# Optimization experiments

Hardware: AMD Instinct MI355X
Metric: run time of the kernel (lower is better)

The kernel has to match this reference:

```python
import jax, jax.numpy as jnp
import numpy as np

B, T, TM, D, H, FF = 4, 1024, 1024, 1024, 16, 4096
HS = D // H
EPS = 1e-5


def _layer_norm(x, g, b):
    m = jnp.mean(x, axis=-1, keepdims=True)
    v = jnp.mean(jnp.square(x - m), axis=-1, keepdims=True)
    return (x - m) / jnp.sqrt(v + EPS) * g + b


def _mha(q_in, k_in, v_in, wq, bq, wk, bk, wv, bv, wo, bo):
    b, t, c = q_in.shape
    tm = k_in.shape[1]
    q = (q_in @ wq + bq).reshape(b, t, H, HS).transpose(0, 2, 1, 3)   # [b,h,t,hs]
    k = (k_in @ wk + bk).reshape(b, tm, H, HS).transpose(0, 2, 1, 3)  # [b,h,tm,hs]
    v = (v_in @ wv + bv).reshape(b, tm, H, HS).transpose(0, 2, 1, 3)
    att = jnp.einsum('bhtd,bhsd->bhts', q, k) * (1.0 / np.sqrt(HS))
    att = jax.nn.softmax(att, axis=-1)                                # [b,h,t,tm]
    y = jnp.einsum('bhts,bhsd->bhtd', att, v)
    y = y.transpose(0, 2, 1, 3).reshape(b, t, c)
    y = y @ wo + bo
    return y, att.mean(axis=1)                                        # attn avg over heads


def setup_inputs() -> dict:
    key = jax.random.key(0)
    ks = jax.random.split(key, 32)
    s = 0.02
    w = lambda k, shape: (jax.random.normal(k, shape, jnp.float32) * s)
    inp = {
        'tgt': jax.random.normal(ks[0], (B, T, D), jnp.float32),
        'memory': jax.random.normal(ks[1], (B, TM, D), jnp.float32),
        # self-attention params
        'sa_wq': w(ks[2], (D, D)), 'sa_bq': jnp.zeros((D,), jnp.float32),
        'sa_wk': w(ks[3], (D, D)), 'sa_bk': jnp.zeros((D,), jnp.float32),
        'sa_wv': w(ks[4], (D, D)), 'sa_bv': jnp.zeros((D,), jnp.float32),
        'sa_wo': w(ks[5], (D, D)), 'sa_bo': jnp.zeros((D,), jnp.float32),
        # cross-attention params
        'ca_wq': w(ks[6], (D, D)), 'ca_bq': jnp.zeros((D,), jnp.float32),
        'ca_wk': w(ks[7], (D, D)), 'ca_bk': jnp.zeros((D,), jnp.float32),
        'ca_wv': w(ks[8], (D, D)), 'ca_bv': jnp.zeros((D,), jnp.float32),
        'ca_wo': w(ks[9], (D, D)), 'ca_bo': jnp.zeros((D,), jnp.float32),
        # FFN
        'w1': w(ks[10], (D, FF)), 'b1': jnp.zeros((FF,), jnp.float32),
        'w2': w(ks[11], (FF, D)), 'b2': jnp.zeros((D,), jnp.float32),
        # LayerNorms
        'ln1_g': jnp.ones((D,), jnp.float32), 'ln1_b': jnp.zeros((D,), jnp.float32),
        'ln2_g': jnp.ones((D,), jnp.float32), 'ln2_b': jnp.zeros((D,), jnp.float32),
        'ln3_g': jnp.ones((D,), jnp.float32), 'ln3_b': jnp.zeros((D,), jnp.float32),
    }
    return inp


def reference(tgt, memory,
              sa_wq, sa_bq, sa_wk, sa_bk, sa_wv, sa_bv, sa_wo, sa_bo,
              ca_wq, ca_bq, ca_wk, ca_bk, ca_wv, ca_bv, ca_wo, ca_bo,
              w1, b1, w2, b2,
              ln1_g, ln1_b, ln2_g, ln2_b, ln3_g, ln3_b):
    x = tgt
    tmp, _ = _mha(x, x, x, sa_wq, sa_bq, sa_wk, sa_bk, sa_wv, sa_bv, sa_wo, sa_bo)
    x = _layer_norm(x + tmp, ln1_g, ln1_b)
    tmp, attention = _mha(x, memory, memory,
                          ca_wq, ca_bq, ca_wk, ca_bk, ca_wv, ca_bv, ca_wo, ca_bo)
    x = _layer_norm(x + tmp, ln2_g, ln2_b)
    tmp = jax.nn.relu(x @ w1 + b1) @ w2 + b2
    x = _layer_norm(x + tmp, ln3_g, ln3_b)
    return x, attention
```

## Files before the change

### kernel.cpp

```cpp
#include <hip/hip_runtime.h>
#include <hip/hip_bf16.h>
#include <cstdint>
#include <cstddef>

using u16 = unsigned short;
typedef __attribute__((ext_vector_type(4))) float f32x4;
typedef __attribute__((ext_vector_type(8))) short bf16x8;
typedef __attribute__((ext_vector_type(4))) short bf16x4;

constexpr int Bc = 4, Tc = 1024, TMc = 1024, Dc = 1024, Hc = 16, HSc = 64, FFc = 4096;
constexpr int BT = Bc * Tc;

struct Ptr4 { u16* p0; u16* p1; u16* p2; u16* p3; };

__device__ __forceinline__ u16 f2bf(float f) {
  union { float f; uint32_t u; } v; v.f = f;
  uint32_t u = v.u;
  u += 0x7fffu + ((u >> 16) & 1u);
  return (u16)(u >> 16);
}
__device__ __forceinline__ u16 f2bf_tr(float f) {
  union { float f; uint32_t u; } v; v.f = f;
  return (u16)(v.u >> 16);
}
__device__ __forceinline__ float b2f(u16 u) {
  union { float f; uint32_t u32; } v; v.u32 = (uint32_t)u << 16; return v.f;
}

__device__ __forceinline__ bf16x8 cat8(bf16x4 lo, bf16x4 hi) {
  bf16x8 r;
  r[0] = lo[0]; r[1] = lo[1]; r[2] = lo[2]; r[3] = lo[3];
  r[4] = hi[0]; r[5] = hi[1]; r[6] = hi[2]; r[7] = hi[3];
  return r;
}

__device__ __forceinline__ void gload16(const u16* g, u16* l) {
  __builtin_amdgcn_global_load_lds((const __attribute__((address_space(1))) void*)g,
                                   (__attribute__((address_space(3))) void*)l, 16, 0, 0);
}

__global__ __launch_bounds__(256)
void tconv(const float* __restrict__ in, u16* __restrict__ outp, int K, int N)
{
  __shared__ u16 tile[64][65];
  const int tx = threadIdx.x & 15, ty = threadIdx.x >> 4;
  const int kb = blockIdx.y * 64, nb = blockIdx.x * 64;
  #pragma unroll
  for (int i = 0; i < 4; ++i) {
    const int r = ty + i * 16;
    const float4 v = *(const float4*)(in + (size_t)(kb + r) * N + nb + tx * 4);
    tile[r][tx * 4 + 0] = f2bf(v.x);
    tile[r][tx * 4 + 1] = f2bf(v.y);
    tile[r][tx * 4 + 2] = f2bf(v.z);
    tile[r][tx * 4 + 3] = f2bf(v.w);
  }
  __syncthreads();
  #pragma unroll
  for (int i = 0; i < 4; ++i) {
    const int n = ty + i * 16;
    bf16x4 o;
    o[0] = (short)tile[tx * 4 + 0][n];
    o[1] = (short)tile[tx * 4 + 1][n];
    o[2] = (short)tile[tx * 4 + 2][n];
    o[3] = (short)tile[tx * 4 + 3][n];
    *(bf16x4*)(outp + (size_t)(nb + n) * K + kb + tx * 4) = o;
  }
}

__global__ __launch_bounds__(256)
void cvt_bf16(const float* __restrict__ in, u16* __restrict__ outp, int n4)
{
  const int i = blockIdx.x * 256 + threadIdx.x;
  if (i < n4) {
    const float4 v = ((const float4*)in)[i];
    bf16x4 o;
    o[0] = (short)f2bf(v.x); o[1] = (short)f2bf(v.y);
    o[2] = (short)f2bf(v.z); o[3] = (short)f2bf(v.w);
    ((bf16x4*)outp)[i] = o;
  }
}

template<int MODE, int BMv, int DEPTH>
__global__ __launch_bounds__((BMv == 256) ? 512 : 256)
void gemm_bt(const u16* __restrict__ A, const u16* __restrict__ Bt,
             const float* __restrict__ bias, const float* __restrict__ resid,
             void* __restrict__ outp, int M, int N, int K, int Kch, Ptr4 P)
{
  constexpr int BM = BMv, BN = 128, BK = 32;
  constexpr int NTHR = (BM == 256) ? 512 : 256;
  constexpr int RPC = NTHR / 4;
  constexpr int ACALLS = BM / RPC;
  constexpr int BCALLS = BN / RPC;
  constexpr int CALLS = ACALLS + BCALLS;
  constexpr int NB = DEPTH + 1;
  __shared__ __align__(16) u16 As[NB][BM * BK];
  __shared__ __align__(16) u16 Bs[NB][BN * BK];
  const int tid = threadIdx.x;
  const int lane = tid & 63, w = tid >> 6;
  const int wr = w >> 1, wc = w & 1;
  const int hi4 = lane >> 4, lr = lane & 15;

  const int nwg = gridDim.x;
  const int GX = N / BN;
  const int bid0 = (int)blockIdx.x;
  const int L = (bid0 & 7) * (nwg >> 3) + (bid0 >> 3);
  const int bandw = 8 * GX;
  const int band = L / bandw;
  const int rem = L - band * bandw;
  const int m0 = (band * 8 + (rem & 7)) * BM;
  const int n0 = (rem >> 3) * BN;

  const int k0 = (MODE == 3) ? (int)blockIdx.y * Kch : 0;

  const int srow = tid >> 2;
  const int gslot = (tid & 3) ^ ((srow >> 1) & 3);
  const u16* ga = A  + (size_t)(m0 + srow) * K + k0 + gslot * 8;
  const u16* gb = Bt + (size_t)(n0 + srow) * K + k0 + gslot * 8;
  const int wofs = w * 512;
  const int cswz = (lr >> 1) & 3;

  auto stage = [&](int buf, int kt) {
    #pragma unroll
    for (int j = 0; j < ACALLS; ++j)
      gload16(ga + (size_t)j * RPC * K + kt, &As[buf][j * NTHR * 8 + wofs]);
    #pragma unroll
    for (int j = 0; j < BCALLS; ++j)
      gload16(gb + (size_t)j * RPC * K + kt, &Bs[buf][j * NTHR * 8 + wofs]);
  };

  f32x4 acc[4][4] = {};
  const int nt = Kch / BK;

  #pragma unroll
  for (int p = 0; p < DEPTH; ++p)
    if (p < nt) stage(p % NB, p * BK);

  int cur = 0;
  for (int t = 0; t < nt; ++t) {
    {
      const int ahead = nt - 1 - t;
      const int cap = (ahead < DEPTH - 1 ? ahead : DEPTH - 1) * CALLS;
      switch (cap) {
        case 0:  asm volatile("s_waitcnt vmcnt(0)"  ::: "memory"); break;
        case 3:  asm volatile("s_waitcnt vmcnt(3)"  ::: "memory"); break;
        case 4:  asm volatile("s_waitcnt vmcnt(4)"  ::: "memory"); break;
        case 8:  asm volatile("s_waitcnt vmcnt(8)"  ::: "memory"); break;
        default: asm volatile("s_waitcnt vmcnt(12)" ::: "memory"); break;
      }
    }
    __builtin_amdgcn_s_barrier();
    __builtin_amdgcn_sched_barrier(0);

    if (t + DEPTH < nt) {
      int b2 = cur + DEPTH; if (b2 >= NB) b2 -= NB;
      stage(b2, (t + DEPTH) * BK);
    }

    bf16x8 af[4], bfr[4];
    #pragma unroll
    for (int mb = 0; mb < 4; ++mb)
      af[mb] = *(const bf16x8*)&As[cur][(wr * 64 + mb * 16 + lr) * BK + (hi4 ^ cswz) * 8];
    #pragma unroll
    for (int nb = 0; nb < 4; ++nb)
      bfr[nb] = *(const bf16x8*)&Bs[cur][(wc * 64 + nb * 16 + lr) * BK + (hi4 ^ cswz) * 8];
    #pragma unroll
    for (int mb = 0; mb < 4; ++mb)
      #pragma unroll
      for (int nb = 0; nb < 4; ++nb)
        acc[mb][nb] = __builtin_amdgcn_mfma_f32_16x16x32_bf16(af[mb], bfr[nb], acc[mb][nb], 0, 0, 0);

    ++cur; if (cur == NB) cur = 0;
  }

  const int orow = m0 + wr * 64 + 4 * hi4;
  const int ocol = n0 + wc * 64 + lr;

  if (MODE == 1) {
    #pragma unroll
    for (int nb = 0; nb < 4; ++nb) {
      const int c = ocol + nb * 16;
      const float bv = bias ? bias[c] : 0.0f;
      #pragma unroll
      for (int mb = 0; mb < 4; ++mb) {
        #pragma unroll
        for (int r = 0; r < 4; ++r) {
          const size_t idx = (size_t)(orow + mb * 16 + r) * N + c;
          ((float*)outp)[idx] = acc[mb][nb][r] + bv + resid[idx];
        }
      }
    }
  } else {
    __syncthreads();
    u16* eb = &Bs[0][0] + w * 1088;
    u16* pout_;
    if (MODE == 3) {
      const int sk = blockIdx.y;
      pout_ = (sk == 0) ? P.p0 : (sk == 1) ? P.p1 : (sk == 2) ? P.p2 : P.p3;
    } else {
      pout_ = (u16*)outp;
    }
    const int r2 = lane >> 3;
    const int c2 = (lane & 7) * 8;
    #pragma unroll
    for (int mb = 0; mb < 4; ++mb) {
      #pragma unroll
      for (int nb = 0; nb < 4; ++nb) {
        const int c = ocol + nb * 16;
        const float bv = (MODE != 3 && bias) ? bias[c] : 0.0f;
        #pragma unroll
        for (int r = 0; r < 4; ++r) {
          float v = acc[mb][nb][r] + bv;
          if (MODE == 2) v = fmaxf(v, 0.0f);
          eb[(4 * hi4 + r) * 68 + nb * 16 + lr] = f2bf(v);
        }
      }
      #pragma unroll
      for (int pass = 0; pass < 2; ++pass) {
        const int rr = pass * 8 + r2;
        const bf16x8 vv = *(const bf16x8*)&eb[rr * 68 + c2];
        *(bf16x8*)&pout_[(size_t)(m0 + wr * 64 + mb * 16 + rr) * N + n0 + wc * 64 + c2] = vv;
      }
    }
  }
}

__global__ __launch_bounds__(256)
void flash_attn(const u16* __restrict__ Q, const u16* __restrict__ Kb,
                const u16* __restrict__ Vb, u16* __restrict__ Y,
                float* __restrict__ Mout, float* __restrict__ Lout,
                int qstr, int kstr)
{
  constexpr int LDK = 72;
  __shared__ __align__(16) u16 Ks[2][64 * LDK];
  __shared__ __align__(16) u16 Vt[2][64 * LDK];
  const int tid = threadIdx.x, lane = tid & 63, w = tid >> 6;
  const int hi4 = lane >> 4, lr = lane & 15;
  const int bh = blockIdx.y, b = bh >> 4, h = bh & 15;
  const int q0 = blockIdx.x * 64 + w * 16;

  bf16x8 qf[2];
  {
    const u16* qp = Q + ((size_t)(b * Tc + q0 + lr)) * qstr + h * HSc;
    #pragma unroll
    for (int ks = 0; ks < 2; ++ks)
      qf[ks] = cat8(*(const bf16x4*)(qp + ks * 32 + 4 * hi4),
                    *(const bf16x4*)(qp + ks * 32 + 16 + 4 * hi4));
  }

  float m_run = -1e30f, l_run = 0.0f;
  f32x4 o[4] = {};

  const int krow = tid >> 3, kcol = (tid & 7) * 8;
  const int s4 = (tid >> 4) * 4;
  const int d4 = (tid & 15) * 4;

  const u16* kbase = Kb + ((size_t)(b * TMc + krow)) * kstr + h * HSc + kcol;
  const u16* vbase = Vb + ((size_t)(b * TMc + s4)) * kstr + h * HSc + d4;

  bf16x8 kreg0, kreg1;
  bf16x4 vreg[4];

  auto loadch = [&](int s0) {
    const u16* kp = kbase + (size_t)s0 * kstr;
    kreg0 = *(const bf16x8*)kp;
    kreg1 = *(const bf16x8*)(kp + (size_t)32 * kstr);
    const u16* vp = vbase + (size_t)s0 * kstr;
    #pragma unroll
    for (int j = 0; j < 4; ++j)
      vreg[j] = *(const bf16x4*)(vp + (size_t)j * kstr);
  };
  auto writech = [&](int buf) {
    *(bf16x8*)&Ks[buf][krow * LDK + kcol]        = kreg0;
    *(bf16x8*)&Ks[buf][(krow + 32) * LDK + kcol] = kreg1;
    #pragma unroll
    for (int i = 0; i < 4; ++i) {
      bf16x4 tr;
      tr[0] = vreg[0][i]; tr[1] = vreg[1][i]; tr[2] = vreg[2][i]; tr[3] = vreg[3][i];
      *(bf16x4*)&Vt[buf][(d4 + i) * LDK + (s4 ^ d4)] = tr;
    }
  };

  loadch(0);
  writech(0);

  constexpr int NT = TMc / 64;
  for (int t = 0; t < NT; ++t) {
    const int cur = t & 1;
    __syncthreads();
    if (t + 1 < NT) loadch((t + 1) * 64);

    f32x4 st[4];
    #pragma unroll
    for (int kb2 = 0; kb2 < 4; ++kb2) {
      f32x4 a = {};
      #pragma unroll
      for (int ks = 0; ks < 2; ++ks) {
        const u16* p = &Ks[cur][(kb2 * 16 + lr) * LDK + ks * 32 + 4 * hi4];
        bf16x8 kf = cat8(*(const bf16x4*)p, *(const bf16x4*)(p + 16));
        a = __builtin_amdgcn_mfma_f32_16x16x32_bf16(kf, qf[ks], a, 0, 0, 0);
      }
      st[kb2] = a;
    }

    float cmax = -1e30f;
    #pragma unroll
    for (int kb2 = 0; kb2 < 4; ++kb2) {
      #pragma unroll
      for (int r = 0; r < 4; ++r) st[kb2][r] *= 0.125f;
      cmax = fmaxf(cmax, fmaxf(fmaxf(st[kb2][0], st[kb2][1]),
                               fmaxf(st[kb2][2], st[kb2][3])));
    }
    cmax = fmaxf(cmax, __shfl_xor(cmax, 16));
    cmax = fmaxf(cmax, __shfl_xor(cmax, 32));

    const bool need = !__all(cmax - m_run <= 8.0f);
    float m_new = m_run, sc = 1.0f;
    if (need) {
      m_new = fmaxf(m_run, cmax);
      sc = __expf(m_run - m_new);
    }
    float psum = 0.0f;
    #pragma unroll
    for (int kb2 = 0; kb2 < 4; ++kb2)
      #pragma unroll
      for (int r = 0; r < 4; ++r) {
        const float e = __expf(st[kb2][r] - m_new);
        st[kb2][r] = e;
        psum += e;
      }
    psum += __shfl_xor(psum, 16);
    psum += __shfl_xor(psum, 32);
    if (need) {
      l_run = l_run * sc + psum;
      #pragma unroll
      for (int r = 0; r < 4; ++r) {
        const float osc = __shfl(sc, 4 * hi4 + r);
        #pragma unroll
        for (int nb = 0; nb < 4; ++nb) o[nb][r] *= osc;
      }
    } else {
      l_run += psum;
    }
    m_run = m_new;

    bf16x8 pa[2];
    #pragma unroll
    for (int ks = 0; ks < 2; ++ks) {
      bf16x8 tv;
      #pragma unroll
      for (int i = 0; i < 4; ++i) tv[i]     = (short)f2bf_tr(st[2 * ks + 0][i]);
      #pragma unroll
      for (int i = 0; i < 4; ++i) tv[4 + i] = (short)f2bf_tr(st[2 * ks + 1][i]);
      pa[ks] = tv;
    }
    #pragma unroll
    for (int nb = 0; nb < 4; ++nb) {
      const int row = nb * 16 + lr;
      const int g = 4 * (row >> 2);
      #pragma unroll
      for (int ks = 0; ks < 2; ++ks) {
        const int c0 = (ks * 32 + 4 * hi4) ^ g;
        const int c1 = (ks * 32 + 16 + 4 * hi4) ^ g;
        bf16x8 vf = cat8(*(const bf16x4*)&Vt[cur][row * LDK + c0],
                         *(const bf16x4*)&Vt[cur][row * LDK + c1]);
        o[nb] = __builtin_amdgcn_mfma_f32_16x16x32_bf16(pa[ks], vf, o[nb], 0, 0, 0);
      }
    }

    if (t + 1 < NT) writech(cur ^ 1);
  }

  #pragma unroll
  for (int r = 0; r < 4; ++r) {
    const float li = 1.0f / __shfl(l_run, 4 * hi4 + r);
    const size_t yr = ((size_t)(b * Tc + q0 + 4 * hi4 + r)) * Dc + h * HSc;
    #pragma unroll
    for (int nb = 0; nb < 4; ++nb)
      Y[yr + nb * 16 + lr] = f2bf(o[nb][r] * li);
  }
  if (Mout != nullptr && lane < 16) {
    Mout[(size_t)bh * Tc + q0 + lr] = m_run;
    Lout[(size_t)bh * Tc + q0 + lr] = l_run;
  }
}

__global__ __launch_bounds__(256)
void attn_avg(const u16* __restrict__ Q, const u16* __restrict__ Kb,
              const float* __restrict__ Mws, const float* __restrict__ Lws,
              float* __restrict__ outp, int qstr, int kstr)
{
  __shared__ __align__(16) u16 Ks[2][64 * 64];
  __shared__ __align__(16) float avg[64 * 68];
  const int tid = threadIdx.x, lane = tid & 63, w = tid >> 6;
  const int hi4 = lane >> 4, lr = lane & 15;
  const int b = blockIdx.z, qt = blockIdx.y, scn = blockIdx.x;
  const int q0 = qt * 64 + w * 16;
  const int s0 = scn * 64;

  const int srow = w * 8 + (lane >> 3);
  const int scol = ((lane & 7) ^ (lane >> 3)) * 8;
  const u16* kg = Kb + ((size_t)(b * TMc + s0 + srow)) * kstr + scol;
  const size_t skip32 = (size_t)32 * kstr;

  auto stage = [&](int buf, int h) {
    const u16* g = kg + h * HSc;
    gload16(g,          &Ks[buf][w * 512]);
    gload16(g + skip32, &Ks[buf][2048 + w * 512]);
  };

  float acc[4][4] = {};
  const int rsw = lr & 7;

  stage(0, 0);
  #pragma unroll 1
  for (int h = 0; h < Hc; ++h) {
    const int cur = h & 1;
    __syncthreads();
    if (h + 1 < Hc) stage(cur ^ 1, h + 1);

    const u16* qp = Q + ((size_t)(b * Tc + q0 + lr)) * qstr + h * HSc;
    const bf16x8 qf0 = *(const bf16x8*)(qp + 8 * hi4);
    const bf16x8 qf1 = *(const bf16x8*)(qp + 32 + 8 * hi4);
    const float mh = Mws[(size_t)(b * Hc + h) * Tc + q0 + lr];
    const float li = 1.0f / Lws[(size_t)(b * Hc + h) * Tc + q0 + lr];

    #pragma unroll
    for (int kb2 = 0; kb2 < 4; ++kb2) {
      const int row = kb2 * 16 + lr;
      const bf16x8 kf0 = *(const bf16x8*)&Ks[cur][row * 64 + ((hi4     ) ^ rsw) * 8];
      const bf16x8 kf1 = *(const bf16x8*)&Ks[cur][row * 64 + ((hi4 + 4) ^ rsw) * 8];
      f32x4 a = {};
      a = __builtin_amdgcn_mfma_f32_16x16x32_bf16(kf0, qf0, a, 0, 0, 0);
      a = __builtin_amdgcn_mfma_f32_16x16x32_bf16(kf1, qf1, a, 0, 0, 0);
      #pragma unroll
      for (int r = 0; r < 4; ++r)
        acc[kb2][r] += __expf(a[r] * 0.125f - mh) * li;
    }
  }

  __syncthreads();
  #pragma unroll
  for (int kb2 = 0; kb2 < 4; ++kb2)
    #pragma unroll
    for (int r = 0; r < 4; ++r)
      avg[(w * 16 + lr) * 68 + kb2 * 16 + 4 * hi4 + r] = acc[kb2][r] * (1.0f / Hc);
  __syncthreads();
  const int row = tid >> 2, col = (tid & 3) * 16;
  float* gp = outp + ((size_t)(b * Tc + qt * 64 + row)) * TMc + s0 + col;
  #pragma unroll
  for (int j = 0; j < 4; ++j)
    *(f32x4*)(gp + j * 4) = *(const f32x4*)&avg[row * 68 + col + j * 4];
}

__global__ __launch_bounds__(256)
void add_ln(const float* __restrict__ in, const float* __restrict__ g,
            const float* __restrict__ bb, float* __restrict__ outf,
            u16* __restrict__ outb)
{
  __shared__ float red1[4];
  __shared__ float red2[4];
  const int tid = threadIdx.x, lane = tid & 63, w = tid >> 6;
  const size_t row = blockIdx.x;
  float4 v = ((const float4*)(in + row * Dc))[tid];
  float s = v.x + v.y + v.z + v.w;
  #pragma unroll
  for (int o = 32; o >= 1; o >>= 1) s += __shfl_xor(s, o);
  if (lane == 0) red1[w] = s;
  __syncthreads();
  s = red1[0] + red1[1] + red1[2] + red1[3];
  const float mean = s * (1.0f / Dc);
  const float dx = v.x - mean, dy = v.y - mean, dz = v.z - mean, dw = v.w - mean;
  float s2 = dx * dx + dy * dy + dz * dz + dw * dw;
  #pragma unroll
  for (int o = 32; o >= 1; o >>= 1) s2 += __shfl_xor(s2, o);
  if (lane == 0) red2[w] = s2;
  __syncthreads();
  s2 = red2[0] + red2[1] + red2[2] + red2[3];
  const float rstd = rsqrtf(s2 * (1.0f / Dc) + 1e-5f);
  const float4 gv = ((const float4*)g)[tid];
  const float4 bv = ((const float4*)bb)[tid];
  float4 o4;
  o4.x = dx * rstd * gv.x + bv.x;
  o4.y = dy * rstd * gv.y + bv.y;
  o4.z = dz * rstd * gv.z + bv.z;
  o4.w = dw * rstd * gv.w + bv.w;
  ((float4*)(outf + row * Dc))[tid] = o4;
  if (outb != nullptr) {
    bf16x4 ob;
    ob[0] = (short)f2bf(o4.x); ob[1] = (short)f2bf(o4.y);
    ob[2] = (short)f2bf(o4.z); ob[3] = (short)f2bf(o4.w);
    *(bf16x4*)(outb + row * Dc + (size_t)tid * 4) = ob;
  }
}

__global__ __launch_bounds__(256)
void add_ln4(const u16* __restrict__ p0, const u16* __restrict__ p1,
             const u16* __restrict__ p2, const u16* __restrict__ p3,
             const float* __restrict__ bias2, const float* __restrict__ resid,
             const float* __restrict__ g, const float* __restrict__ bb,
             float* __restrict__ outf)
{
  __shared__ float red1[4];
  __shared__ float red2[4];
  const int tid = threadIdx.x, lane = tid & 63, w = tid >> 6;
  const size_t row = blockIdx.x;
  const size_t base = row * Dc + (size_t)tid * 4;
  const bf16x4 a0 = *(const bf16x4*)(p0 + base);
  const bf16x4 a1 = *(const bf16x4*)(p1 + base);
  const bf16x4 a2 = *(const bf16x4*)(p2 + base);
  const bf16x4 a3 = *(const bf16x4*)(p3 + base);
  const float4 rv = ((const float4*)(resid + row * Dc))[tid];
  const float4 b2 = ((const float4*)bias2)[tid];
  float4 v;
  v.x = b2f((u16)a0[0]) + b2f((u16)a1[0]) + b2f((u16)a2[0]) + b2f((u16)a3[0]) + b2.x + rv.x;
  v.y = b2f((u16)a0[1]) + b2f((u16)a1[1]) + b2f((u16)a2[1]) + b2f((u16)a3[1]) + b2.y + rv.y;
  v.z = b2f((u16)a0[2]) + b2f((u16)a1[2]) + b2f((u16)a2[2]) + b2f((u16)a3[2]) + b2.z + rv.z;
  v.w = b2f((u16)a0[3]) + b2f((u16)a1[3]) + b2f((u16)a2[3]) + b2f((u16)a3[3]) + b2.w + rv.w;
  float s = v.x + v.y + v.z + v.w;
  #pragma unroll
  for (int o = 32; o >= 1; o >>= 1) s += __shfl_xor(s, o);
  if (lane == 0) red1[w] = s;
  __syncthreads();
  s = red1[0] + red1[1] + red1[2] + red1[3];
  const float mean = s * (1.0f / Dc);
  const float dx = v.x - mean, dy = v.y - mean, dz = v.z - mean, dw = v.w - mean;
  float s2 = dx * dx + dy * dy + dz * dz + dw * dw;
  #pragma unroll
  for (int o = 32; o >= 1; o >>= 1) s2 += __shfl_xor(s2, o);
  if (lane == 0) red2[w] = s2;
  __syncthreads();
  s2 = red2[0] + red2[1] + red2[2] + red2[3];
  const float rstd = rsqrtf(s2 * (1.0f / Dc) + 1e-5f);
  const float4 gv = ((const float4*)g)[tid];
  const float4 bv = ((const float4*)bb)[tid];
  float4 o4;
  o4.x = dx * rstd * gv.x + bv.x;
  o4.y = dy * rstd * gv.y + bv.y;
  o4.z = dz * rstd * gv.z + bv.z;
  o4.w = dw * rstd * gv.w + bv.w;
  ((float4*)(outf + row * Dc))[tid] = o4;
}

extern "C" void kernel_launch(void* const* d_in, const int* in_sizes, int n_in,
                              void* d_out, int out_size, void* d_ws, size_t ws_size,
                              hipStream_t stream)
{
  (void)in_sizes; (void)n_in; (void)out_size; (void)ws_size;
  const float* tgt = (const float*)d_in[0];
  const float* mem = (const float*)d_in[1];
  const float* Wf[10]   = { (const float*)d_in[2],  (const float*)d_in[4],  (const float*)d_in[6],  (const float*)d_in[8],
                            (const float*)d_in[10], (const float*)d_in[12], (const float*)d_in[14], (const float*)d_in[16],
                            (const float*)d_in[18], (const float*)d_in[20] };
  const float* bias_[10]= { (const float*)d_in[3],  (const float*)d_in[5],  (const float*)d_in[7],  (const float*)d_in[9],
                            (const float*)d_in[11], (const float*)d_in[13], (const float*)d_in[15], (const float*)d_in[17],
                            (const float*)d_in[19], (const float*)d_in[21] };
  const float* ln1g = (const float*)d_in[22]; const float* ln1b = (const float*)d_in[23];
  const float* ln2g = (const float*)d_in[24]; const float* ln2b = (const float*)d_in[25];
  const float* ln3g = (const float*)d_in[26]; const float* ln3b = (const float*)d_in[27];

  char* wsp = (char*)d_ws;
  auto alloc = [&](size_t bytes) -> char* {
    char* p = wsp;
    wsp += (bytes + 255) & ~(size_t)255;
    return p;
  };
  u16* wT[8];
  for (int i = 0; i < 8; ++i) wT[i] = (u16*)alloc((size_t)Dc * Dc * 2);
  u16* w1T  = (u16*)alloc((size_t)Dc * FFc * 2);
  u16* w2T  = (u16*)alloc((size_t)Dc * FFc * 2);
  u16* xb   = (u16*)alloc((size_t)BT * Dc * 2);
  u16* memb = (u16*)alloc((size_t)BT * Dc * 2);
  u16* qb   = (u16*)alloc((size_t)BT * Dc * 2);
  u16* yb   = (u16*)alloc((size_t)BT * Dc * 2);
  u16* ffb  = (u16*)alloc((size_t)BT * FFc * 2);
  float* res = (float*)alloc((size_t)BT * Dc * 4);
  float* xf  = (float*)alloc((size_t)BT * Dc * 4);
  float* mws = (float*)alloc((size_t)Bc * Hc * Tc * 4);
  float* lws = (float*)alloc((size_t)Bc * Hc * Tc * 4);
  float* bqkv = (float*)alloc(3 * Dc * 4);
  float* bkv  = (float*)alloc(2 * Dc * 4);

  u16* qkv    = ffb;
  u16* kvb    = ffb;
  u16* wqkvT  = (u16*)res;
  Ptr4 fp { qb, yb, memb, (u16*)res };

  float* out_x   = (float*)d_out;
  float* out_att = out_x + (size_t)BT * Dc;

  Ptr4 z { nullptr, nullptr, nullptr, nullptr };

  for (int i = 0; i < 8; ++i)
    tconv<<<dim3(Dc / 64, Dc / 64), 256, 0, stream>>>(Wf[i], wT[i], Dc, Dc);
  tconv<<<dim3(FFc / 64, Dc / 64), 256, 0, stream>>>(Wf[8], w1T, Dc, FFc);
  tconv<<<dim3(Dc / 64, FFc / 64), 256, 0, stream>>>(Wf[9], w2T, FFc, Dc);
  cvt_bf16<<<BT * Dc / 4 / 256, 256, 0, stream>>>(tgt, xb, BT * Dc / 4);
  cvt_bf16<<<BT * Dc / 4 / 256, 256, 0, stream>>>(mem, memb, BT * Dc / 4);

  for (int j = 0; j < 3; ++j) {
    hipMemcpyAsync(wqkvT + (size_t)j * Dc * Dc, wT[j], (size_t)Dc * Dc * 2,
                   hipMemcpyDeviceToDevice, stream);
    hipMemcpyAsync(bqkv + j * Dc, bias_[j], Dc * 4, hipMemcpyDeviceToDevice, stream);
  }
  for (int j = 0; j < 2; ++j)
    hipMemcpyAsync(bkv + j * Dc, bias_[5 + j], Dc * 4, hipMemcpyDeviceToDevice, stream);

  const int nD    = (Dc / 128) * (BT / 128);
  const int nQKVw = (3 * Dc / 128) * (BT / 256);
  const int nKVw  = (2 * Dc / 128) * (BT / 256);
  const int nFw   = (FFc / 128) * (BT / 256);
  const dim3 gAtt(Tc / 64, Bc * Hc);
  const dim3 gAvg(TMc / 64, Tc / 64, Bc);

  gemm_bt<0, 256, 2><<<nQKVw, 512, 0, stream>>>(xb, wqkvT, bqkv, nullptr, qkv, BT, 3 * Dc, Dc, Dc, z);
  flash_attn<<<gAtt, 256, 0, stream>>>(qkv, qkv + Dc, qkv + 2 * Dc, yb,
                                       nullptr, nullptr, 3 * Dc, 3 * Dc);
  gemm_bt<1, 128, 2><<<nD, 256, 0, stream>>>(yb, wT[3], bias_[3], tgt, res, BT, Dc, Dc, Dc, z);
  add_ln<<<BT, 256, 0, stream>>>(res, ln1g, ln1b, xf, xb);

  gemm_bt<0, 128, 2><<<nD, 256, 0, stream>>>(xb, wT[4], bias_[4], nullptr, qb, BT, Dc, Dc, Dc, z);
  gemm_bt<0, 256, 2><<<nKVw, 512, 0, stream>>>(memb, wT[5], bkv, nullptr, kvb, BT, 2 * Dc, Dc, Dc, z);
  flash_attn<<<gAtt, 256, 0, stream>>>(qb, kvb, kvb + Dc, yb, mws, lws, Dc, 2 * Dc);
  attn_avg<<<gAvg, 256, 0, stream>>>(qb, kvb, mws, lws, out_att, Dc, 2 * Dc);
  gemm_bt<1, 128, 2><<<nD, 256, 0, stream>>>(yb, wT[7], bias_[7], xf, res, BT, Dc, Dc, Dc, z);
  add_ln<<<BT, 256, 0, stream>>>(res, ln2g, ln2b, xf, xb);

  gemm_bt<2, 256, 2><<<nFw, 512, 0, stream>>>(xb,  w1T, bias_[8], nullptr, ffb, BT, FFc, Dc, Dc, z);
  gemm_bt<3, 128, 2><<<dim3(nD, 4), 256, 0, stream>>>(ffb, w2T, nullptr, nullptr, nullptr,
                                                      BT, Dc, FFc, FFc / 4, fp);
  add_ln4<<<BT, 256, 0, stream>>>(fp.p0, fp.p1, fp.p2, fp.p3, bias_[9], xf,
                                  ln3g, ln3b, out_x);
}
```

Before: 452.6 us.

## Batch weight transposes, replace memcpys with bias kernel, use exp2 softmax

Combines the eight square weight transposes into one launch that writes the Q/K/V weights straight into the concatenated buffer, and replaces eight device-to-device memcpys with a single bias concatenation kernel. The flash attention and attention-average kernels switch to base-2 exponentials with a pre-scaled constant and a matching rescale threshold. Probability packing to bf16 now uses a byte-permute instruction, two values at a time. The saved M statistic is now in base-2 units, so the attention-average kernel must agree with the flash kernel; both were changed together.

```diff
diff --git a/kernel.cpp b/kernel.cpp
--- a/kernel.cpp
+++ b/kernel.cpp
@@ -10,8 +10,11 @@
 
 constexpr int Bc = 4, Tc = 1024, TMc = 1024, Dc = 1024, Hc = 16, HSc = 64, FFc = 4096;
 constexpr int BT = Bc * Tc;
+constexpr float C2 = 0.18033688f;
 
 struct Ptr4 { u16* p0; u16* p1; u16* p2; u16* p3; };
+struct P8f  { const float* p[8]; };
+struct P8u  { u16* p[8]; };
 
 __device__ __forceinline__ u16 f2bf(float f) {
   union { float f; uint32_t u; } v; v.f = f;
@@ -19,12 +22,12 @@
   u += 0x7fffu + ((u >> 16) & 1u);
   return (u16)(u >> 16);
 }
-__device__ __forceinline__ u16 f2bf_tr(float f) {
-  union { float f; uint32_t u; } v; v.f = f;
-  return (u16)(v.u >> 16);
-}
 __device__ __forceinline__ float b2f(u16 u) {
   union { float f; uint32_t u32; } v; v.u32 = (uint32_t)u << 16; return v.f;
+}
+__device__ __forceinline__ uint32_t pk2(float hi, float lo) {
+  union { float f; uint32_t u; } a, b; a.f = hi; b.f = lo;
+  return __builtin_amdgcn_perm(a.u, b.u, 0x07060302u);
 }
 
 __device__ __forceinline__ bf16x8 cat8(bf16x4 lo, bf16x4 hi) {
@@ -37,6 +40,36 @@
 __device__ __forceinline__ void gload16(const u16* g, u16* l) {
   __builtin_amdgcn_global_load_lds((const __attribute__((address_space(1))) void*)g,
                                    (__attribute__((address_space(3))) void*)l, 16, 0, 0);
+}
+
+__global__ __launch_bounds__(256)
+void tconv8(P8f S, P8u D)
+{
+  __shared__ u16 tile[64][65];
+  const float* in = S.p[blockIdx.z];
+  u16* outp = D.p[blockIdx.z];
+  const int tx = threadIdx.x & 15, ty = threadIdx.x >> 4;
+  const int kb = blockIdx.y * 64, nb = blockIdx.x * 64;
+  #pragma unroll
+  for (int i = 0; i < 4; ++i) {
+    const int r = ty + i * 16;
+    const float4 v = *(const float4*)(in + (size_t)(kb + r) * Dc + nb + tx * 4);
+    tile[r][tx * 4 + 0] = f2bf(v.x);
+    tile[r][tx * 4 + 1] = f2bf(v.y);
+    tile[r][tx * 4 + 2] = f2bf(v.z);
+    tile[r][tx * 4 + 3] = f2bf(v.w);
+  }
+  __syncthreads();
+  #pragma unroll
+  for (int i = 0; i < 4; ++i) {
+    const int n = ty + i * 16;
+    bf16x4 o;
+    o[0] = (short)tile[tx * 4 + 0][n];
+    o[1] = (short)tile[tx * 4 + 1][n];
+    o[2] = (short)tile[tx * 4 + 2][n];
+    o[3] = (short)tile[tx * 4 + 3][n];
+    *(bf16x4*)(outp + (size_t)(nb + n) * Dc + kb + tx * 4) = o;
+  }
 }
 
 __global__ __launch_bounds__(256)
@@ -77,6 +110,21 @@
     o[0] = (short)f2bf(v.x); o[1] = (short)f2bf(v.y);
     o[2] = (short)f2bf(v.z); o[3] = (short)f2bf(v.w);
     ((bf16x4*)outp)[i] = o;
+  }
+}
+
+__global__ __launch_bounds__(1024)
+void biascat(float* __restrict__ bqkv, float* __restrict__ bkv,
+             const float* b0, const float* b1, const float* b2,
+             const float* b5, const float* b6)
+{
+  const int t = threadIdx.x, z = blockIdx.x;
+  if (z < 3) {
+    const float* s = (z == 0) ? b0 : (z == 1) ? b1 : b2;
+    bqkv[z * 1024 + t] = s[t];
+  } else {
+    const float* s = (z == 3) ? b5 : b6;
+    bkv[(z - 3) * 1024 + t] = s[t];
   }
 }
 
@@ -306,25 +354,25 @@
     #pragma unroll
     for (int kb2 = 0; kb2 < 4; ++kb2) {
       #pragma unroll
-      for (int r = 0; r < 4; ++r) st[kb2][r] *= 0.125f;
+      for (int r = 0; r < 4; ++r) st[kb2][r] *= C2;
       cmax = fmaxf(cmax, fmaxf(fmaxf(st[kb2][0], st[kb2][1]),
                                fmaxf(st[kb2][2], st[kb2][3])));
     }
     cmax = fmaxf(cmax, __shfl_xor(cmax, 16));
     cmax = fmaxf(cmax, __shfl_xor(cmax, 32));
 
-    const bool need = !__all(cmax - m_run <= 8.0f);
+    const bool need = !__all(cmax - m_run <= 11.5416f);
     float m_new = m_run, sc = 1.0f;
     if (need) {
       m_new = fmaxf(m_run, cmax);
-      sc = __expf(m_run - m_new);
+      sc = exp2f(m_run - m_new);
     }
     float psum = 0.0f;
     #pragma unroll
     for (int kb2 = 0; kb2 < 4; ++kb2)
       #pragma unroll
       for (int r = 0; r < 4; ++r) {
-        const float e = __expf(st[kb2][r] - m_new);
+        const float e = exp2f(st[kb2][r] - m_new);
         st[kb2][r] = e;
         psum += e;
       }
@@ -346,12 +394,12 @@
     bf16x8 pa[2];
     #pragma unroll
     for (int ks = 0; ks < 2; ++ks) {
-      bf16x8 tv;
-      #pragma unroll
-      for (int i = 0; i < 4; ++i) tv[i]     = (short)f2bf_tr(st[2 * ks + 0][i]);
-      #pragma unroll
-      for (int i = 0; i < 4; ++i) tv[4 + i] = (short)f2bf_tr(st[2 * ks + 1][i]);
-      pa[ks] = tv;
+      union { bf16x8 v; uint32_t u[4]; } pw;
+      pw.u[0] = pk2(st[2 * ks + 0][1], st[2 * ks + 0][0]);
+      pw.u[1] = pk2(st[2 * ks + 0][3], st[2 * ks + 0][2]);
+      pw.u[2] = pk2(st[2 * ks + 1][1], st[2 * ks + 1][0]);
+      pw.u[3] = pk2(st[2 * ks + 1][3], st[2 * ks + 1][2]);
+      pa[ks] = pw.v;
     }
     #pragma unroll
     for (int nb = 0; nb < 4; ++nb) {
@@ -421,7 +469,7 @@
     const u16* qp = Q + ((size_t)(b * Tc + q0 + lr)) * qstr + h * HSc;
     const bf16x8 qf0 = *(const bf16x8*)(qp + 8 * hi4);
     const bf16x8 qf1 = *(const bf16x8*)(qp + 32 + 8 * hi4);
-    const float mh = Mws[(size_t)(b * Hc + h) * Tc + q0 + lr];
+    const float mh2 = Mws[(size_t)(b * Hc + h) * Tc + q0 + lr];
     const float li = 1.0f / Lws[(size_t)(b * Hc + h) * Tc + q0 + lr];
 
     #pragma unroll
@@ -434,7 +482,7 @@
       a = __builtin_amdgcn_mfma_f32_16x16x32_bf16(kf1, qf1, a, 0, 0, 0);
       #pragma unroll
       for (int r = 0; r < 4; ++r)
-        acc[kb2][r] += __expf(a[r] * 0.125f - mh) * li;
+        acc[kb2][r] += exp2f(a[r] * C2 - mh2) * li;
     }
   }
 
@@ -590,20 +638,20 @@
 
   Ptr4 z { nullptr, nullptr, nullptr, nullptr };
 
-  for (int i = 0; i < 8; ++i)
-    tconv<<<dim3(Dc / 64, Dc / 64), 256, 0, stream>>>(Wf[i], wT[i], Dc, Dc);
+  {
+    P8f S; P8u D;
+    for (int i = 0; i < 8; ++i) S.p[i] = Wf[i];
+    D.p[0] = wqkvT;               D.p[1] = wqkvT + (size_t)Dc * Dc;
+    D.p[2] = wqkvT + (size_t)2 * Dc * Dc;
+    for (int i = 3; i < 8; ++i) D.p[i] = wT[i];
+    tconv8<<<dim3(16, 16, 8), 256, 0, stream>>>(S, D);
+  }
   tconv<<<dim3(FFc / 64, Dc / 64), 256, 0, stream>>>(Wf[8], w1T, Dc, FFc);
   tconv<<<dim3(Dc / 64, FFc / 64), 256, 0, stream>>>(Wf[9], w2T, FFc, Dc);
   cvt_bf16<<<BT * Dc / 4 / 256, 256, 0, stream>>>(tgt, xb, BT * Dc / 4);
   cvt_bf16<<<BT * Dc / 4 / 256, 256, 0, stream>>>(mem, memb, BT * Dc / 4);
-
-  for (int j = 0; j < 3; ++j) {
-    hipMemcpyAsync(wqkvT + (size_t)j * Dc * Dc, wT[j], (size_t)Dc * Dc * 2,
-                   hipMemcpyDeviceToDevice, stream);
-    hipMemcpyAsync(bqkv + j * Dc, bias_[j], Dc * 4, hipMemcpyDeviceToDevice, stream);
-  }
-  for (int j = 0; j < 2; ++j)
-    hipMemcpyAsync(bkv + j * Dc, bias_[5 + j], Dc * 4, hipMemcpyDeviceToDevice, stream);
+  biascat<<<5, 1024, 0, stream>>>(bqkv, bkv, bias_[0], bias_[1], bias_[2],
+                                  bias_[5], bias_[6]);
 
   const int nD    = (Dc / 128) * (BT / 128);
   const int nQKVw = (3 * Dc / 128) * (BT / 256);
```

New measurement: 433.2 us. -4.3%, faster.
